# Optimization experiments

Measured on AMD Instinct MI355X. Metric: run time of the kernel, lower is better.

## Reference

```python
import jax, jax.numpy as jnp
import numpy as np

V_TH = 1.0  # spikingjelly IFNode default threshold; v starts at 0, hard reset after fire


def setup_inputs() -> dict:
    key = jax.random.key(0)
    k_x, k_w1, k_w2 = jax.random.split(key, 3)
    B, IN, FEAT, OUT = 4096, 3136, 6272, 500
    # binary input spikes (LatencyEncoder emits 0/1 spikes per timestep)
    x = (jax.random.uniform(k_x, (B, IN)) < 0.5).astype(jnp.float32)
    # Linear weights, torch layout [out_features, in_features], kaiming-ish scale
    W1 = jax.random.normal(k_w1, (FEAT, IN), dtype=jnp.float32) / np.sqrt(IN)
    W2 = jax.random.normal(k_w2, (OUT, FEAT), dtype=jnp.float32) / np.sqrt(FEAT)
    return {"x": x, "W1": W1, "W2": W2}


def reference(x, W1, W2):
    # Linear (no bias) -> IF neuron single step: v = 0 + I; spike = (v >= V_TH); hard reset
    v1 = x @ W1.T                      # [B, FEAT]
    s1 = (v1 >= V_TH).astype(x.dtype)  # binary hidden spikes
    v2 = s1 @ W2.T                     # [B, OUT]
    s2 = (v2 >= V_TH).astype(x.dtype)  # output spikes
    return s2
```

## Files before the change

### kernel.cpp

```cpp
#include <hip/hip_runtime.h>


namespace {
constexpr int kB = 4096;
constexpr int kIn = 3136;
constexpr int kFeat = 6272;
constexpr int kFeatWords = 196;
constexpr int kOut = 500;
constexpr size_t kPlane1 = (size_t)kFeat * kIn;
constexpr size_t kW1F = 3 * kPlane1;
constexpr size_t kW2F = (size_t)784 * 12288;
constexpr size_t kS1Bytes = (size_t)kB * kFeatWords * 4;
constexpr size_t kXb2Bytes = (size_t)49 * kB * 8;
constexpr unsigned kCap1 = 2u << 20;
constexpr unsigned kCap2 = 1u << 16;
__device__ constexpr double kTau1 = 7.4769e-4;
__device__ constexpr double kTau2 = 1.4955e-3;
}

typedef int v4i __attribute__((ext_vector_type(4)));
typedef int v16i __attribute__((ext_vector_type(16)));

__device__ __forceinline__ void gload_lds16(const void* g, void* l) {
  __builtin_amdgcn_global_load_lds((__attribute__((address_space(1))) void*)(g),
                                   (__attribute__((address_space(3))) void*)(l),
                                   16, 0, 0);
}

__device__ __forceinline__ v4i expand16(unsigned b) {
  unsigned u0 = (((b      ) & 0xFu) * 0x204081u) & 0x01010101u;
  unsigned u1 = (((b >> 4 ) & 0xFu) * 0x204081u) & 0x01010101u;
  unsigned u2 = (((b >> 8 ) & 0xFu) * 0x204081u) & 0x01010101u;
  unsigned u3 = (((b >> 12) & 0xFu) * 0x204081u) & 0x01010101u;
  return (v4i){(int)u0, (int)u1, (int)u2, (int)u3};
}

__device__ __forceinline__ void split3(float w, signed char* d) {
  float c = rintf(w * 128.f);
  d[0] = (signed char)(int)c;
  float r = fmaf(c, -7.8125e-03f, w);
  c = rintf(r * 16384.f);
  d[1] = (signed char)(int)c;
  r = fmaf(c, -6.103515625e-05f, r);
  c = rintf(r * 2097152.f);
  d[2] = (signed char)(int)c;
}

__global__ __launch_bounds__(256) void conv_w1F(const float* __restrict__ W,
                                                signed char* __restrict__ F) {
  const int bx = blockIdx.x;
  const int fb = bx / 49;
  const int kt = bx % 49;
  const int f = threadIdx.x & 63;
  const int g = threadIdx.x >> 6;
  const float* src = W + (size_t)(fb * 64 + f) * kIn + kt * 64 + g * 16;
  union { signed char c[16]; int4 v; } o[3];
#pragma unroll
  for (int q = 0; q < 4; ++q) {
    const float4 w = *(const float4*)(src + q * 4);
    signed char d[4][3];
    split3(w.x, d[0]); split3(w.y, d[1]); split3(w.z, d[2]); split3(w.w, d[3]);
#pragma unroll
    for (int e = 0; e < 4; ++e)
#pragma unroll
      for (int j = 0; j < 3; ++j) o[j].c[q * 4 + e] = d[e][j];
  }
#pragma unroll
  for (int j = 0; j < 3; ++j)
    *(int4*)(F + ((size_t)bx * 3 + j) * 4096 + g * 1024 + f * 16) = o[j].v;
}

__global__ __launch_bounds__(256) void conv_w2F(const float* __restrict__ W,
                                                signed char* __restrict__ F) {
  const int bx = blockIdx.x;
  const int fb = bx / 98;
  const int kt = bx % 98;
  const int f = threadIdx.x & 63;
  const int g = threadIdx.x >> 6;
  const int feat = fb * 64 + f;
  union { signed char c[16]; int4 v; } o[3];
#pragma unroll
  for (int q = 0; q < 4; ++q) {
    float4 w = {0.f, 0.f, 0.f, 0.f};
    if (feat < kOut)
      w = *(const float4*)(W + (size_t)feat * kFeat + kt * 64 + g * 16 + q * 4);
    signed char d[4][3];
    split3(w.x, d[0]); split3(w.y, d[1]); split3(w.z, d[2]); split3(w.w, d[3]);
#pragma unroll
    for (int e = 0; e < 4; ++e)
#pragma unroll
      for (int j = 0; j < 3; ++j) o[j].c[q * 4 + e] = d[e][j];
  }
#pragma unroll
  for (int j = 0; j < 3; ++j)
    *(int4*)(F + ((size_t)bx * 3 + j) * 4096 + g * 1024 + f * 16) = o[j].v;
}

__global__ __launch_bounds__(256) void pack_x2(const float* __restrict__ X,
                                               uint2* __restrict__ xb2) {
  const int wid = (blockIdx.x * 256 + threadIdx.x) >> 6;
  const int lane = threadIdx.x & 63;
  const int b = wid / 49;
  const int g = wid % 49;
  const float v = X[(size_t)b * kIn + g * 64 + lane];
  const unsigned long long bal = __ballot(v != 0.f);
  if (lane == 0) xb2[(size_t)g * kB + b] = make_uint2((unsigned)bal, (unsigned)(bal >> 32));
}

__global__ __launch_bounds__(512, 4) void fc1_v6(
    const uint2* __restrict__ xb2, const signed char* __restrict__ w1lF,
    unsigned* __restrict__ s1b, unsigned* __restrict__ s1T,
    unsigned* __restrict__ cnt, unsigned* __restrict__ list) {
  __shared__ __align__(16) signed char lds[24576];
  const int tid = threadIdx.x;
  const int lane = tid & 63;
  const int ln31 = lane & 31;
  const int half = lane >> 5;
  const int wv = tid >> 6;
  const int waveM = wv >> 1;
  const int waveN = wv & 1;
  const int bx = blockIdx.y;
  const int bM = blockIdx.x * 128;

  const signed char* const gbase = w1lF + (size_t)bx * 49 * 12288;
  const bool has1 = (wv < 4);
  const unsigned sG0 = wv * 1024u + lane * 16u;
  const unsigned sL0 = wv * 1024u;
  const unsigned sG1 = (wv + 8) * 1024u + lane * 16u;
  const unsigned sL1 = (wv + 8) * 1024u;

  const uint2* const aptr = xb2 + bM + waveM * 32 + ln31;
  const unsigned bfeat = (waveN * 32 + ln31) * 16u;

  v16i acc[3] = {};
  uint2 aC, aN;
  aC = aptr[0];
  gload_lds16(gbase + sG0, lds + sL0);
  if (has1) gload_lds16(gbase + sG1, lds + sL1);

  for (int kt = 0; kt < 49; ++kt) {
    __syncthreads();
    const int cb = (kt & 1) * 12288;
    if (kt < 48) {
      const int nb = ((kt + 1) & 1) * 12288;
      const size_t go = (size_t)(kt + 1) * 12288;
      gload_lds16(gbase + go + sG0, lds + nb + sL0);
      if (has1) gload_lds16(gbase + go + sG1, lds + nb + sL1);
      aN = aptr[(size_t)(kt + 1) * kB];
    }
#pragma unroll
    for (int kk = 0; kk < 2; ++kk) {
      const unsigned gsel = (kk * 2 + half) * 1024u;
      const v4i b0 = *(const v4i*)(lds + cb + 0 * 4096 + gsel + bfeat);
      const v4i b1 = *(const v4i*)(lds + cb + 1 * 4096 + gsel + bfeat);
      const v4i b2 = *(const v4i*)(lds + cb + 2 * 4096 + gsel + bfeat);
      const unsigned word = kk ? aC.y : aC.x;
      const v4i a = expand16((word >> (half * 16)) & 0xFFFFu);
      acc[0] = __builtin_amdgcn_mfma_i32_32x32x32_i8(a, b0, acc[0], 0, 0, 0);
      acc[1] = __builtin_amdgcn_mfma_i32_32x32x32_i8(a, b1, acc[1], 0, 0, 0);
      acc[2] = __builtin_amdgcn_mfma_i32_32x32x32_i8(a, b2, acc[2], 0, 0, 0);
    }
    aC = aN;
  }

  const double s7 = 0.0078125;
  const int word = bx * 2 + waveN;
  const int fcol = word * 32 + ln31;
#pragma unroll
  for (int t = 0; t < 16; ++t) {
    double v = (double)acc[2][t];
    v = v * s7 + (double)acc[1][t];
    v = v * s7 + (double)acc[0][t];
    v = v * s7;
    const unsigned long long bal = __ballot(v >= 1.0);
    const int mrow = bM + waveM * 32 + (t & 3) + 8 * (t >> 2);
    if (lane == 0) {
      s1b[(size_t)mrow * kFeatWords + word] = (unsigned)bal;
      s1T[(size_t)word * kB + mrow] = (unsigned)bal;
    }
    if (lane == 32) {
      s1b[(size_t)(mrow + 4) * kFeatWords + word] = (unsigned)(bal >> 32);
      s1T[(size_t)word * kB + mrow + 4] = (unsigned)(bal >> 32);
    }
    if (fabs(v - 1.0) <= kTau1) {
      const unsigned idx = atomicAdd(cnt, 1u);
      if (idx < kCap1) list[idx] = ((unsigned)(mrow + 4 * half) << 13) | (unsigned)fcol;
    }
  }
}

__global__ __launch_bounds__(256) void fc1_correct(
    const float* __restrict__ x, const float* __restrict__ W1,
    const unsigned* __restrict__ cnt, const unsigned* __restrict__ list,
    unsigned* __restrict__ s1b, unsigned* __restrict__ s1T) {
  const unsigned n = min(cnt[0], kCap1);
  const int lane = threadIdx.x & 63;
  const int wid = (blockIdx.x * 256 + threadIdx.x) >> 6;
  const int nw = (gridDim.x * 256) >> 6;
  for (unsigned i = wid; i < n; i += nw) {
    const unsigned u = list[i];
    const int b = (int)(u >> 13);
    const int f = (int)(u & 8191u);
    double s = 0.0;
    for (int k = lane; k < kIn; k += 64)
      s = fma((double)x[(size_t)b * kIn + k], (double)W1[(size_t)f * kIn + k], s);
#pragma unroll
    for (int off = 32; off > 0; off >>= 1) s += __shfl_down(s, off);
    if (lane == 0) {
      const unsigned mask = 1u << (f & 31);
      unsigned* p1 = s1b + (size_t)b * kFeatWords + (f >> 5);
      unsigned* p2 = s1T + (size_t)(f >> 5) * kB + b;
      if (s >= 1.0) { atomicOr(p1, mask); atomicOr(p2, mask); }
      else          { atomicAnd(p1, ~mask); atomicAnd(p2, ~mask); }
    }
  }
}

__global__ __launch_bounds__(128, 4) void fc2_v6(
    const unsigned* __restrict__ s1T, const signed char* __restrict__ w2lF,
    float* __restrict__ out, unsigned* __restrict__ cnt,
    unsigned* __restrict__ list) {
  const int tid = threadIdx.x;
  const int lane = tid & 63;
  const int ln31 = lane & 31;
  const int half = lane >> 5;
  const int wvN = tid >> 6;
  const int bx = blockIdx.y;
  const int bM = blockIdx.x * 32;

  const unsigned* const aptr = s1T + bM + ln31;
  const int fl = wvN * 32 + ln31;
  const signed char* const bbase =
      w2lF + (size_t)(bx * 98) * 12288 + half * 1024u + fl * 16u;

  v16i acc[3] = {};
  v4i b0[6], b1[6];
  uint2 a0, a1;

#define LOAD_TILE(nk, bf, ab)                                   \
  {                                                             \
    const signed char* bp = bbase + (size_t)(nk) * 12288;       \
    bf[0] = *(const v4i*)(bp);                                  \
    bf[1] = *(const v4i*)(bp + 2048);                           \
    bf[2] = *(const v4i*)(bp + 4096);                           \
    bf[3] = *(const v4i*)(bp + 6144);                           \
    bf[4] = *(const v4i*)(bp + 8192);                           \
    bf[5] = *(const v4i*)(bp + 10240);                          \
    (ab).x = aptr[(size_t)((nk) * 2) * kB];                     \
    (ab).y = aptr[(size_t)((nk) * 2 + 1) * kB];                 \
  }
#define COMPUTE_TILE(bf, ab)                                                    \
  {                                                                             \
    _Pragma("unroll")                                                           \
    for (int kk = 0; kk < 2; ++kk) {                                            \
      const unsigned word = kk ? (ab).y : (ab).x;                               \
      const v4i a = expand16((word >> (half * 16)) & 0xFFFFu);                  \
      acc[0] = __builtin_amdgcn_mfma_i32_32x32x32_i8(a, bf[kk], acc[0], 0,0,0); \
      acc[1] = __builtin_amdgcn_mfma_i32_32x32x32_i8(a, bf[2+kk], acc[1],0,0,0);\
      acc[2] = __builtin_amdgcn_mfma_i32_32x32x32_i8(a, bf[4+kk], acc[2],0,0,0);\
    }                                                                           \
  }

  LOAD_TILE(0, b0, a0);
  for (int kt = 0; kt + 2 <= 98; kt += 2) {
    LOAD_TILE(kt + 1, b1, a1);
    COMPUTE_TILE(b0, a0);
    const int nk2 = (kt + 2 < 98) ? kt + 2 : 97;
    LOAD_TILE(nk2, b0, a0);
    COMPUTE_TILE(b1, a1);
  }

  const double s7 = 0.0078125;
  const int o = bx * 64 + wvN * 32 + ln31;
#pragma unroll
  for (int t = 0; t < 16; ++t) {
    double v = (double)acc[2][t];
    v = v * s7 + (double)acc[1][t];
    v = v * s7 + (double)acc[0][t];
    v = v * s7;
    const int b = bM + (t & 3) + 8 * (t >> 2) + 4 * half;
    if (o < kOut) {
      out[(size_t)b * kOut + o] = (v >= 1.0) ? 1.0f : 0.0f;
      if (fabs(v - 1.0) <= kTau2) {
        const unsigned idx = atomicAdd(cnt, 1u);
        if (idx < kCap2) list[idx] = ((unsigned)b << 13) | (unsigned)o;
      }
    }
  }
#undef LOAD_TILE
#undef COMPUTE_TILE
}

__global__ __launch_bounds__(256) void fc2_correct(
    const unsigned* __restrict__ s1b, const float* __restrict__ W2,
    const unsigned* __restrict__ cnt, const unsigned* __restrict__ list,
    float* __restrict__ out) {
  const unsigned n = min(cnt[0], kCap2);
  const int lane = threadIdx.x & 63;
  const int wid = (blockIdx.x * 256 + threadIdx.x) >> 6;
  const int nw = (gridDim.x * 256) >> 6;
  for (unsigned i = wid; i < n; i += nw) {
    const unsigned u = list[i];
    const int b = (int)(u >> 13);
    const int o = (int)(u & 8191u);
    double s = 0.0;
    for (int k = lane; k < kFeat; k += 64) {
      const unsigned w = s1b[(size_t)b * kFeatWords + (k >> 5)];
      if ((w >> (k & 31)) & 1u) s += (double)W2[(size_t)o * kFeat + k];
    }
#pragma unroll
    for (int off = 32; off > 0; off >>= 1) s += __shfl_down(s, off);
    if (lane == 0) out[(size_t)b * kOut + o] = (s >= 1.0) ? 1.0f : 0.0f;
  }
}

__global__ __launch_bounds__(256) void snn_fc1(const float* __restrict__ x,
                                               const float* __restrict__ W1,
                                               unsigned int* __restrict__ s1bits) {
  __shared__ double Xd[32][66];
  __shared__ double Wd[32][66];
  __shared__ unsigned int spikes[64][2];
  const int tid = threadIdx.x;
  const int tx = tid & 15;
  const int ty = tid >> 4;
  const int b0 = blockIdx.y * 64;
  const int f0 = blockIdx.x * 64;
  if (tid < 128) spikes[tid >> 1][tid & 1] = 0u;
  double acc[4][4];
#pragma unroll
  for (int j = 0; j < 4; ++j)
#pragma unroll
    for (int i = 0; i < 4; ++i) acc[j][i] = 0.0;
  const int rl = tid >> 2;
  const int kq = (tid & 3) * 8;
  const float* xrow = x + (size_t)(b0 + rl) * kIn + kq;
  const float* wrow = W1 + (size_t)(f0 + rl) * kIn + kq;
  for (int kc = 0; kc < kIn; kc += 32) {
    const float4 xv0 = *(const float4*)(xrow + kc);
    const float4 xv1 = *(const float4*)(xrow + kc + 4);
    const float4 wv0 = *(const float4*)(wrow + kc);
    const float4 wv1 = *(const float4*)(wrow + kc + 4);
    __syncthreads();
    Xd[kq + 0][rl] = (double)xv0.x; Xd[kq + 1][rl] = (double)xv0.y;
    Xd[kq + 2][rl] = (double)xv0.z; Xd[kq + 3][rl] = (double)xv0.w;
    Xd[kq + 4][rl] = (double)xv1.x; Xd[kq + 5][rl] = (double)xv1.y;
    Xd[kq + 6][rl] = (double)xv1.z; Xd[kq + 7][rl] = (double)xv1.w;
    Wd[kq + 0][rl] = (double)wv0.x; Wd[kq + 1][rl] = (double)wv0.y;
    Wd[kq + 2][rl] = (double)wv0.z; Wd[kq + 3][rl] = (double)wv0.w;
    Wd[kq + 4][rl] = (double)wv1.x; Wd[kq + 5][rl] = (double)wv1.y;
    Wd[kq + 6][rl] = (double)wv1.z; Wd[kq + 7][rl] = (double)wv1.w;
    __syncthreads();
#pragma unroll
    for (int k = 0; k < 32; ++k) {
      const double2 xa = *(const double2*)&Xd[k][ty * 4];
      const double2 xb = *(const double2*)&Xd[k][ty * 4 + 2];
      const double2 wa = *(const double2*)&Wd[k][tx * 4];
      const double2 wb = *(const double2*)&Wd[k][tx * 4 + 2];
      const double xv[4] = {xa.x, xa.y, xb.x, xb.y};
      const double wv[4] = {wa.x, wa.y, wb.x, wb.y};
#pragma unroll
      for (int j = 0; j < 4; ++j)
#pragma unroll
        for (int i = 0; i < 4; ++i) acc[j][i] += xv[j] * wv[i];
    }
  }
  __syncthreads();
#pragma unroll
  for (int j = 0; j < 4; ++j) {
    unsigned int nib = 0u;
#pragma unroll
    for (int i = 0; i < 4; ++i) nib |= (acc[j][i] >= 1.0 ? 1u : 0u) << i;
    atomicOr(&spikes[ty * 4 + j][tx >> 3], nib << ((tx * 4) & 31));
  }
  __syncthreads();
  if (tid < 128) {
    const int r = tid >> 1;
    const int w = tid & 1;
    s1bits[(size_t)(b0 + r) * kFeatWords + (f0 >> 5) + w] = spikes[r][w];
  }
}

__global__ __launch_bounds__(256) void snn_fc2(const unsigned int* __restrict__ s1bits,
                                               const float* __restrict__ W2,
                                               float* __restrict__ out) {
  __shared__ double Wd[32][66];
  __shared__ unsigned int Sb[64];
  const int tid = threadIdx.x;
  const int tx = tid & 15;
  const int ty = tid >> 4;
  const int b0 = blockIdx.y * 64;
  const int o0 = blockIdx.x * 64;
  double acc[4][4];
#pragma unroll
  for (int j = 0; j < 4; ++j)
#pragma unroll
    for (int i = 0; i < 4; ++i) acc[j][i] = 0.0;
  const int rl = tid >> 2;
  const int kq = (tid & 3) * 8;
  int orow = o0 + rl;
  if (orow >= kOut) orow = kOut - 1;
  const float* wrow = W2 + (size_t)orow * kFeat + kq;
  for (int kc = 0; kc < kFeat; kc += 32) {
    const float4 wv0 = *(const float4*)(wrow + kc);
    const float4 wv1 = *(const float4*)(wrow + kc + 4);
    unsigned int sword = 0u;
    if (tid < 64) sword = s1bits[(size_t)(b0 + tid) * kFeatWords + (kc >> 5)];
    __syncthreads();
    Wd[kq + 0][rl] = (double)wv0.x; Wd[kq + 1][rl] = (double)wv0.y;
    Wd[kq + 2][rl] = (double)wv0.z; Wd[kq + 3][rl] = (double)wv0.w;
    Wd[kq + 4][rl] = (double)wv1.x; Wd[kq + 5][rl] = (double)wv1.y;
    Wd[kq + 6][rl] = (double)wv1.z; Wd[kq + 7][rl] = (double)wv1.w;
    if (tid < 64) Sb[tid] = sword;
    __syncthreads();
    const unsigned int rw0 = Sb[ty * 4 + 0];
    const unsigned int rw1 = Sb[ty * 4 + 1];
    const unsigned int rw2 = Sb[ty * 4 + 2];
    const unsigned int rw3 = Sb[ty * 4 + 3];
#pragma unroll
    for (int k = 0; k < 32; ++k) {
      const double2 wa = *(const double2*)&Wd[k][tx * 4];
      const double2 wb = *(const double2*)&Wd[k][tx * 4 + 2];
      const double wv[4] = {wa.x, wa.y, wb.x, wb.y};
      const double sv[4] = {(double)((rw0 >> k) & 1u), (double)((rw1 >> k) & 1u),
                            (double)((rw2 >> k) & 1u), (double)((rw3 >> k) & 1u)};
#pragma unroll
      for (int j = 0; j < 4; ++j)
#pragma unroll
        for (int i = 0; i < 4; ++i) acc[j][i] += sv[j] * wv[i];
    }
  }
#pragma unroll
  for (int j = 0; j < 4; ++j) {
    const int b = b0 + ty * 4 + j;
#pragma unroll
    for (int i = 0; i < 4; ++i) {
      const int o = o0 + tx * 4 + i;
      if (o < kOut) out[(size_t)b * kOut + o] = (acc[j][i] >= 1.0) ? 1.0f : 0.0f;
    }
  }
}

extern "C" void kernel_launch(void* const* d_in, const int* in_sizes, int n_in,
                              void* d_out, int out_size, void* d_ws, size_t ws_size,
                              hipStream_t stream) {
  const float* x = (const float*)d_in[0];
  const float* W1 = (const float*)d_in[1];
  const float* W2 = (const float*)d_in[2];
  float* out = (float*)d_out;

  char* p = (char*)d_ws;
  signed char* w1lF = (signed char*)p;   p += kW1F;
  signed char* w2lF = (signed char*)p;   p += kW2F;
  unsigned* s1b = (unsigned*)p;          p += kS1Bytes;
  unsigned* s1T = (unsigned*)p;          p += kS1Bytes;
  uint2* xb2 = (uint2*)p;                p += kXb2Bytes;
  unsigned* list1 = (unsigned*)p;        p += (size_t)kCap1 * 4;
  unsigned* list2 = (unsigned*)p;        p += (size_t)kCap2 * 4;
  unsigned* ctrs = (unsigned*)p;         p += 256;
  const size_t need = (size_t)(p - (char*)d_ws);

  if (ws_size >= need) {
    hipMemsetAsync(ctrs, 0, 32, stream);
    conv_w1F<<<4802, 256, 0, stream>>>(W1, w1lF);
    conv_w2F<<<784, 256, 0, stream>>>(W2, w2lF);
    pack_x2<<<50176, 256, 0, stream>>>(x, xb2);
    fc1_v6<<<dim3(32, 98), 512, 0, stream>>>(xb2, w1lF, s1b, s1T, ctrs, list1);
    fc1_correct<<<1024, 256, 0, stream>>>(x, W1, ctrs, list1, s1b, s1T);
    fc2_v6<<<dim3(128, 8), 128, 0, stream>>>(s1T, w2lF, out, ctrs + 4, list2);
    fc2_correct<<<64, 256, 0, stream>>>(s1b, W2, ctrs + 4, list2, out);
  } else {
    unsigned* s1 = (unsigned*)d_ws;
    snn_fc1<<<dim3(98, 64), 256, 0, stream>>>(x, W1, s1);
    snn_fc2<<<dim3(8, 64), 256, 0, stream>>>(s1, W2, out);
  }
}
```

Baseline: 585.7 us.

## Triple-buffer fc1 LDS pipeline with manual waitcnt and swizzle block order

Rewrites the fc1 main loop to use three LDS stages instead of two, issuing loads two tiles ahead and using explicit vmcnt waits plus a raw s_barrier instead of __syncthreads at the top of each iteration. It also raises MFMA issue priority with s_setprio and remaps block indices in both fc1 and fc2 so that consecutive blocks are spread across weight column tiles, aiming for better L2/XCD locality. The goal is to hide global-to-LDS latency and cut barrier stalls. In exchange it uses more LDS per block, which may reduce occupancy, and the hand-written wait counts are fragile.

```diff
diff --git a/kernel.cpp b/kernel.cpp
--- a/kernel.cpp
+++ b/kernel.cpp
@@ -107,11 +107,11 @@
   if (lane == 0) xb2[(size_t)g * kB + b] = make_uint2((unsigned)bal, (unsigned)(bal >> 32));
 }
 
-__global__ __launch_bounds__(512, 4) void fc1_v6(
+__global__ __launch_bounds__(512, 4) void fc1_v7(
     const uint2* __restrict__ xb2, const signed char* __restrict__ w1lF,
     unsigned* __restrict__ s1b, unsigned* __restrict__ s1T,
     unsigned* __restrict__ cnt, unsigned* __restrict__ list) {
-  __shared__ __align__(16) signed char lds[24576];
+  __shared__ __align__(16) signed char lds[36864];
   const int tid = threadIdx.x;
   const int lane = tid & 63;
   const int ln31 = lane & 31;
@@ -119,8 +119,11 @@
   const int wv = tid >> 6;
   const int waveM = wv >> 1;
   const int waveN = wv & 1;
-  const int bx = blockIdx.y;
-  const int bM = blockIdx.x * 128;
+
+  const int lin = blockIdx.x + 32 * blockIdx.y;
+  const int sw = (lin & 7) * 392 + (lin >> 3);
+  const int bx = sw >> 5;
+  const int bM = (sw & 31) * 128;
 
   const signed char* const gbase = w1lF + (size_t)bx * 49 * 12288;
   const bool has1 = (wv < 4);
@@ -134,34 +137,74 @@
 
   v16i acc[3] = {};
   uint2 aC, aN;
+
+#define FC1_TILE(CBC, AA)                                                     \
+  {                                                                           \
+    _Pragma("unroll")                                                         \
+    for (int kk = 0; kk < 2; ++kk) {                                          \
+      const unsigned gsel = (kk * 2 + half) * 1024u;                          \
+      const v4i b0 = *(const v4i*)(lds + (CBC) + 0 * 4096 + gsel + bfeat);    \
+      const v4i b1 = *(const v4i*)(lds + (CBC) + 1 * 4096 + gsel + bfeat);    \
+      const v4i b2 = *(const v4i*)(lds + (CBC) + 2 * 4096 + gsel + bfeat);    \
+      const unsigned word = kk ? (AA).y : (AA).x;                             \
+      const v4i a = expand16((word >> (half * 16)) & 0xFFFFu);                \
+      __builtin_amdgcn_s_setprio(1);                                          \
+      acc[0] = __builtin_amdgcn_mfma_i32_32x32x32_i8(a, b0, acc[0], 0, 0, 0); \
+      acc[1] = __builtin_amdgcn_mfma_i32_32x32x32_i8(a, b1, acc[1], 0, 0, 0); \
+      acc[2] = __builtin_amdgcn_mfma_i32_32x32x32_i8(a, b2, acc[2], 0, 0, 0); \
+      __builtin_amdgcn_s_setprio(0);                                          \
+    }                                                                         \
+  }
+
+#define FC1_STEP(CBC, SBC, AUSE, ALOAD)                                       \
+  {                                                                           \
+    ALOAD = *apre;                                                            \
+    apre += kB;                                                               \
+    gload_lds16(gstage + sG0, lds + (SBC) + sL0);                             \
+    if (has1) gload_lds16(gstage + sG1, lds + (SBC) + sL1);                   \
+    gstage += 12288;                                                          \
+    FC1_TILE(CBC, AUSE);                                                      \
+    if (has1) asm volatile("s_waitcnt vmcnt(3)" ::: "memory");                \
+    else      asm volatile("s_waitcnt vmcnt(2)" ::: "memory");                \
+    __builtin_amdgcn_s_barrier();                                             \
+    asm volatile("" ::: "memory");                                            \
+  }
+
   aC = aptr[0];
+  asm volatile("" ::: "memory");
   gload_lds16(gbase + sG0, lds + sL0);
   if (has1) gload_lds16(gbase + sG1, lds + sL1);
-
-  for (int kt = 0; kt < 49; ++kt) {
-    __syncthreads();
-    const int cb = (kt & 1) * 12288;
-    if (kt < 48) {
-      const int nb = ((kt + 1) & 1) * 12288;
-      const size_t go = (size_t)(kt + 1) * 12288;
-      gload_lds16(gbase + go + sG0, lds + nb + sL0);
-      if (has1) gload_lds16(gbase + go + sG1, lds + nb + sL1);
-      aN = aptr[(size_t)(kt + 1) * kB];
-    }
-#pragma unroll
-    for (int kk = 0; kk < 2; ++kk) {
-      const unsigned gsel = (kk * 2 + half) * 1024u;
-      const v4i b0 = *(const v4i*)(lds + cb + 0 * 4096 + gsel + bfeat);
-      const v4i b1 = *(const v4i*)(lds + cb + 1 * 4096 + gsel + bfeat);
-      const v4i b2 = *(const v4i*)(lds + cb + 2 * 4096 + gsel + bfeat);
-      const unsigned word = kk ? aC.y : aC.x;
-      const v4i a = expand16((word >> (half * 16)) & 0xFFFFu);
-      acc[0] = __builtin_amdgcn_mfma_i32_32x32x32_i8(a, b0, acc[0], 0, 0, 0);
-      acc[1] = __builtin_amdgcn_mfma_i32_32x32x32_i8(a, b1, acc[1], 0, 0, 0);
-      acc[2] = __builtin_amdgcn_mfma_i32_32x32x32_i8(a, b2, acc[2], 0, 0, 0);
-    }
-    aC = aN;
-  }
+  gload_lds16(gbase + 12288 + sG0, lds + 12288 + sL0);
+  if (has1) gload_lds16(gbase + 12288 + sG1, lds + 12288 + sL1);
+  if (has1) asm volatile("s_waitcnt vmcnt(2)" ::: "memory");
+  else      asm volatile("s_waitcnt vmcnt(1)" ::: "memory");
+  __builtin_amdgcn_s_barrier();
+  asm volatile("" ::: "memory");
+
+  const uint2* apre = aptr + (size_t)kB;
+  const signed char* gstage = gbase + 2 * 12288;
+
+  for (int t = 0; t < 7; ++t) {
+    FC1_STEP(0,     24576, aC, aN);
+    FC1_STEP(12288, 0,     aN, aC);
+    FC1_STEP(24576, 12288, aC, aN);
+    FC1_STEP(0,     24576, aN, aC);
+    FC1_STEP(12288, 0,     aC, aN);
+    FC1_STEP(24576, 12288, aN, aC);
+  }
+  FC1_STEP(0,     24576, aC, aN);
+  FC1_STEP(12288, 0,     aN, aC);
+  FC1_STEP(24576, 12288, aC, aN);
+  FC1_STEP(0,     24576, aN, aC);
+  FC1_STEP(12288, 0,     aC, aN);
+  aC = *apre;
+  FC1_TILE(24576, aN);
+  asm volatile("s_waitcnt vmcnt(0)" ::: "memory");
+  __builtin_amdgcn_s_barrier();
+  asm volatile("" ::: "memory");
+  FC1_TILE(0, aC);
+
+#undef FC1_STEP
 
   const double s7 = 0.0078125;
   const int word = bx * 2 + waveN;
@@ -187,6 +230,7 @@
       if (idx < kCap1) list[idx] = ((unsigned)(mrow + 4 * half) << 13) | (unsigned)fcol;
     }
   }
+#undef FC1_TILE
 }
 
 __global__ __launch_bounds__(256) void fc1_correct(
@@ -216,7 +260,7 @@
   }
 }
 
-__global__ __launch_bounds__(128, 4) void fc2_v6(
+__global__ __launch_bounds__(128, 4) void fc2_v7(
     const unsigned* __restrict__ s1T, const signed char* __restrict__ w2lF,
     float* __restrict__ out, unsigned* __restrict__ cnt,
     unsigned* __restrict__ list) {
@@ -225,8 +269,11 @@
   const int ln31 = lane & 31;
   const int half = lane >> 5;
   const int wvN = tid >> 6;
-  const int bx = blockIdx.y;
-  const int bM = blockIdx.x * 32;
+
+  const int lin = blockIdx.x + 128 * blockIdx.y;
+  const int sw = ((lin & 7) << 7) + (lin >> 3);
+  const int bx = sw >> 7;
+  const int bM = (sw & 127) * 32;
 
   const unsigned* const aptr = s1T + bM + ln31;
   const int fl = wvN * 32 + ln31;
@@ -464,9 +511,9 @@
     conv_w1F<<<4802, 256, 0, stream>>>(W1, w1lF);
     conv_w2F<<<784, 256, 0, stream>>>(W2, w2lF);
     pack_x2<<<50176, 256, 0, stream>>>(x, xb2);
-    fc1_v6<<<dim3(32, 98), 512, 0, stream>>>(xb2, w1lF, s1b, s1T, ctrs, list1);
+    fc1_v7<<<dim3(32, 98), 512, 0, stream>>>(xb2, w1lF, s1b, s1T, ctrs, list1);
     fc1_correct<<<1024, 256, 0, stream>>>(x, W1, ctrs, list1, s1b, s1T);
-    fc2_v6<<<dim3(128, 8), 128, 0, stream>>>(s1T, w2lF, out, ctrs + 4, list2);
+    fc2_v7<<<dim3(128, 8), 128, 0, stream>>>(s1T, w2lF, out, ctrs + 4, list2);
     fc2_correct<<<64, 256, 0, stream>>>(s1b, W2, ctrs + 4, list2, out);
   } else {
     unsigned* s1 = (unsigned*)d_ws;
```

After: 588.0 us. No clear change (+0.4%).

## Deepen fc1 LDS pipeline to four stages and swizzle block order

Applied to the files above, without the earlier changes.

fc1 now uses a 4-buffer LDS ring with three tiles in flight, in place of a double buffer with a full __syncthreads each step. It uses explicit vmcnt waits, raw barriers, and register prefetch of the next B fragments so LDS reads overlap the MFMAs. Both fc1 and fc2 remap their linear block index with a swizzle so that concurrently running blocks are spread across XCD-interleaved tiles, aiming at better L2 reuse. The change doubles LDS per block, which may lower occupancy. The hand-written waitcnt counts are fragile if the compiler reorders memory ops.

```diff
diff --git a/kernel.cpp b/kernel.cpp
--- a/kernel.cpp
+++ b/kernel.cpp
@@ -107,11 +107,11 @@
   if (lane == 0) xb2[(size_t)g * kB + b] = make_uint2((unsigned)bal, (unsigned)(bal >> 32));
 }
 
-__global__ __launch_bounds__(512, 4) void fc1_v6(
+__global__ __launch_bounds__(512, 4) void fc1_v8(
     const uint2* __restrict__ xb2, const signed char* __restrict__ w1lF,
     unsigned* __restrict__ s1b, unsigned* __restrict__ s1T,
     unsigned* __restrict__ cnt, unsigned* __restrict__ list) {
-  __shared__ __align__(16) signed char lds[24576];
+  __shared__ __align__(16) signed char lds[49152];
   const int tid = threadIdx.x;
   const int lane = tid & 63;
   const int ln31 = lane & 31;
@@ -119,8 +119,11 @@
   const int wv = tid >> 6;
   const int waveM = wv >> 1;
   const int waveN = wv & 1;
-  const int bx = blockIdx.y;
-  const int bM = blockIdx.x * 128;
+
+  const int lin = blockIdx.x + 32 * blockIdx.y;
+  const int sw = (lin & 7) * 392 + (lin >> 3);
+  const int bx = sw >> 5;
+  const int bM = (sw & 31) * 128;
 
   const signed char* const gbase = w1lF + (size_t)bx * 49 * 12288;
   const bool has1 = (wv < 4);
@@ -131,37 +134,82 @@
 
   const uint2* const aptr = xb2 + bM + waveM * 32 + ln31;
   const unsigned bfeat = (waveN * 32 + ln31) * 16u;
+  const unsigned g0sel = half * 1024u;
+  const unsigned g1sel = (2 + half) * 1024u;
 
   v16i acc[3] = {};
+  v4i bA0, bA1, bA2;
+  v4i bB0, bB1, bB2;
   uint2 aC, aN;
+
+#define FC1_PHASE(CB, PB, SB, AU, AL, SOFF, AOFF, DO_STAGE, DO_A, DO_PRE, WAITM) \
+  {                                                                           \
+    bB0 = *(const v4i*)(lds + (CB) + 0 * 4096 + g1sel + bfeat);               \
+    bB1 = *(const v4i*)(lds + (CB) + 1 * 4096 + g1sel + bfeat);               \
+    bB2 = *(const v4i*)(lds + (CB) + 2 * 4096 + g1sel + bfeat);               \
+    if (DO_STAGE) {                                                           \
+      gload_lds16(gstage + (SOFF) + sG0, lds + (SB) + sL0);                   \
+      if (has1) gload_lds16(gstage + (SOFF) + sG1, lds + (SB) + sL1);         \
+    }                                                                         \
+    if (DO_A) { (AL) = apre[(size_t)(AOFF)]; }                                \
+    {                                                                         \
+      const v4i a0 = expand16(((AU).x >> (half * 16)) & 0xFFFFu);             \
+      acc[0] = __builtin_amdgcn_mfma_i32_32x32x32_i8(a0, bA0, acc[0], 0,0,0); \
+      acc[1] = __builtin_amdgcn_mfma_i32_32x32x32_i8(a0, bA1, acc[1], 0,0,0); \
+      acc[2] = __builtin_amdgcn_mfma_i32_32x32x32_i8(a0, bA2, acc[2], 0,0,0); \
+      const v4i a1 = expand16(((AU).y >> (half * 16)) & 0xFFFFu);             \
+      acc[0] = __builtin_amdgcn_mfma_i32_32x32x32_i8(a1, bB0, acc[0], 0,0,0); \
+      acc[1] = __builtin_amdgcn_mfma_i32_32x32x32_i8(a1, bB1, acc[1], 0,0,0); \
+      acc[2] = __builtin_amdgcn_mfma_i32_32x32x32_i8(a1, bB2, acc[2], 0,0,0); \
+    }                                                                         \
+    if (DO_PRE) {                                                             \
+      bA0 = *(const v4i*)(lds + (PB) + 0 * 4096 + g0sel + bfeat);             \
+      bA1 = *(const v4i*)(lds + (PB) + 1 * 4096 + g0sel + bfeat);             \
+      bA2 = *(const v4i*)(lds + (PB) + 2 * 4096 + g0sel + bfeat);             \
+    }                                                                         \
+    if ((WAITM) == 0) {                                                       \
+      if (has1) asm volatile("s_waitcnt vmcnt(3)" ::: "memory");              \
+      else      asm volatile("s_waitcnt vmcnt(2)" ::: "memory");              \
+      __builtin_amdgcn_s_barrier();                                           \
+      asm volatile("" ::: "memory");                                          \
+    } else if ((WAITM) == 1) {                                                \
+      asm volatile("s_waitcnt vmcnt(2)" ::: "memory");                        \
+      __builtin_amdgcn_s_barrier();                                           \
+      asm volatile("" ::: "memory");                                          \
+    }                                                                         \
+  }
+
+  gload_lds16(gbase + 0 * 12288 + sG0, lds + 0 + sL0);
+  if (has1) gload_lds16(gbase + 0 * 12288 + sG1, lds + 0 + sL1);
+  gload_lds16(gbase + 1 * 12288 + sG0, lds + 12288 + sL0);
+  if (has1) gload_lds16(gbase + 1 * 12288 + sG1, lds + 12288 + sL1);
+  gload_lds16(gbase + 2 * 12288 + sG0, lds + 24576 + sL0);
+  if (has1) gload_lds16(gbase + 2 * 12288 + sG1, lds + 24576 + sL1);
   aC = aptr[0];
-  gload_lds16(gbase + sG0, lds + sL0);
-  if (has1) gload_lds16(gbase + sG1, lds + sL1);
-
-  for (int kt = 0; kt < 49; ++kt) {
-    __syncthreads();
-    const int cb = (kt & 1) * 12288;
-    if (kt < 48) {
-      const int nb = ((kt + 1) & 1) * 12288;
-      const size_t go = (size_t)(kt + 1) * 12288;
-      gload_lds16(gbase + go + sG0, lds + nb + sL0);
-      if (has1) gload_lds16(gbase + go + sG1, lds + nb + sL1);
-      aN = aptr[(size_t)(kt + 1) * kB];
-    }
-#pragma unroll
-    for (int kk = 0; kk < 2; ++kk) {
-      const unsigned gsel = (kk * 2 + half) * 1024u;
-      const v4i b0 = *(const v4i*)(lds + cb + 0 * 4096 + gsel + bfeat);
-      const v4i b1 = *(const v4i*)(lds + cb + 1 * 4096 + gsel + bfeat);
-      const v4i b2 = *(const v4i*)(lds + cb + 2 * 4096 + gsel + bfeat);
-      const unsigned word = kk ? aC.y : aC.x;
-      const v4i a = expand16((word >> (half * 16)) & 0xFFFFu);
-      acc[0] = __builtin_amdgcn_mfma_i32_32x32x32_i8(a, b0, acc[0], 0, 0, 0);
-      acc[1] = __builtin_amdgcn_mfma_i32_32x32x32_i8(a, b1, acc[1], 0, 0, 0);
-      acc[2] = __builtin_amdgcn_mfma_i32_32x32x32_i8(a, b2, acc[2], 0, 0, 0);
-    }
-    aC = aN;
-  }
+  asm volatile("s_waitcnt vmcnt(0)" ::: "memory");
+  __builtin_amdgcn_s_barrier();
+  asm volatile("" ::: "memory");
+  bA0 = *(const v4i*)(lds + 0 * 4096 + g0sel + bfeat);
+  bA1 = *(const v4i*)(lds + 1 * 4096 + g0sel + bfeat);
+  bA2 = *(const v4i*)(lds + 2 * 4096 + g0sel + bfeat);
+
+  const uint2* apre = aptr + (size_t)kB;
+  const signed char* gstage = gbase + 3 * 12288;
+
+  for (int t = 0; t < 11; ++t) {
+    FC1_PHASE(0,     12288, 36864, aC, aN, 0,         0,      1, 1, 1, 0);
+    FC1_PHASE(12288, 24576, 0,     aN, aC, 12288,     kB,     1, 1, 1, 0);
+    FC1_PHASE(24576, 36864, 12288, aC, aN, 2 * 12288, 2 * kB, 1, 1, 1, 0);
+    FC1_PHASE(36864, 0,     24576, aN, aC, 3 * 12288, 3 * kB, 1, 1, 1, 0);
+    gstage += 4 * 12288;
+    apre += (size_t)4 * kB;
+  }
+  FC1_PHASE(0,     12288, 36864, aC, aN, 0,     0,      1, 1, 1, 0);
+  FC1_PHASE(12288, 24576, 0,     aN, aC, 12288, kB,     1, 1, 1, 0);
+  FC1_PHASE(24576, 36864, 0,     aC, aN, 0,     2 * kB, 0, 1, 1, 1);
+  FC1_PHASE(36864, 0,     0,     aN, aC, 0,     3 * kB, 0, 1, 1, 2);
+  FC1_PHASE(0,     0,     0,     aC, aN, 0,     0,      0, 0, 0, 2);
+#undef FC1_PHASE
 
   const double s7 = 0.0078125;
   const int word = bx * 2 + waveN;
@@ -216,7 +264,7 @@
   }
 }
 
-__global__ __launch_bounds__(128, 4) void fc2_v6(
+__global__ __launch_bounds__(128, 4) void fc2_v7(
     const unsigned* __restrict__ s1T, const signed char* __restrict__ w2lF,
     float* __restrict__ out, unsigned* __restrict__ cnt,
     unsigned* __restrict__ list) {
@@ -225,8 +273,11 @@
   const int ln31 = lane & 31;
   const int half = lane >> 5;
   const int wvN = tid >> 6;
-  const int bx = blockIdx.y;
-  const int bM = blockIdx.x * 32;
+
+  const int lin = blockIdx.x + 128 * blockIdx.y;
+  const int sw = ((lin & 7) << 7) + (lin >> 3);
+  const int bx = sw >> 7;
+  const int bM = (sw & 127) * 32;
 
   const unsigned* const aptr = s1T + bM + ln31;
   const int fl = wvN * 32 + ln31;
@@ -464,9 +515,9 @@
     conv_w1F<<<4802, 256, 0, stream>>>(W1, w1lF);
     conv_w2F<<<784, 256, 0, stream>>>(W2, w2lF);
     pack_x2<<<50176, 256, 0, stream>>>(x, xb2);
-    fc1_v6<<<dim3(32, 98), 512, 0, stream>>>(xb2, w1lF, s1b, s1T, ctrs, list1);
+    fc1_v8<<<dim3(32, 98), 512, 0, stream>>>(xb2, w1lF, s1b, s1T, ctrs, list1);
     fc1_correct<<<1024, 256, 0, stream>>>(x, W1, ctrs, list1, s1b, s1T);
-    fc2_v6<<<dim3(128, 8), 128, 0, stream>>>(s1T, w2lF, out, ctrs + 4, list2);
+    fc2_v7<<<dim3(128, 8), 128, 0, stream>>>(s1T, w2lF, out, ctrs + 4, list2);
     fc2_correct<<<64, 256, 0, stream>>>(s1b, W2, ctrs + 4, list2, out);
   } else {
     unsigned* s1 = (unsigned*)d_ws;
```

New measurement: 587.0 us. No clear change (+0.2%).

## Stage three K-tiles per barrier in fc1 and swizzle block order in fc1/fc2

Applied to the files above, without the earlier changes.

The fc1 kernel now loads three 12 KB weight K-tiles into a larger double-buffered LDS region per iteration, cutting the number of barriers from 49 to 17 and issuing more async global-to-LDS loads per barrier. Both fc1 and fc2 remap their linear block index with a swizzle so that concurrently running blocks on different XCDs share weight or activation tiles, aiming for better L2 reuse. The larger LDS allocation (72 KB) may lower occupancy below the declared launch bound of 4 blocks.

```diff
diff --git a/kernel.cpp b/kernel.cpp
--- a/kernel.cpp
+++ b/kernel.cpp
@@ -107,11 +107,11 @@
   if (lane == 0) xb2[(size_t)g * kB + b] = make_uint2((unsigned)bal, (unsigned)(bal >> 32));
 }
 
-__global__ __launch_bounds__(512, 4) void fc1_v6(
+__global__ __launch_bounds__(512, 4) void fc1_v9(
     const uint2* __restrict__ xb2, const signed char* __restrict__ w1lF,
     unsigned* __restrict__ s1b, unsigned* __restrict__ s1T,
     unsigned* __restrict__ cnt, unsigned* __restrict__ list) {
-  __shared__ __align__(16) signed char lds[24576];
+  __shared__ __align__(16) signed char lds[73728];
   const int tid = threadIdx.x;
   const int lane = tid & 63;
   const int ln31 = lane & 31;
@@ -119,49 +119,83 @@
   const int wv = tid >> 6;
   const int waveM = wv >> 1;
   const int waveN = wv & 1;
-  const int bx = blockIdx.y;
-  const int bM = blockIdx.x * 128;
+
+  const int lin = blockIdx.x + 32 * blockIdx.y;
+  const int sw = (lin & 7) * 392 + (lin >> 3);
+  const int bx = sw >> 5;
+  const int bM = (sw & 31) * 128;
 
   const signed char* const gbase = w1lF + (size_t)bx * 49 * 12288;
-  const bool has1 = (wv < 4);
   const unsigned sG0 = wv * 1024u + lane * 16u;
   const unsigned sL0 = wv * 1024u;
-  const unsigned sG1 = (wv + 8) * 1024u + lane * 16u;
-  const unsigned sL1 = (wv + 8) * 1024u;
 
   const uint2* const aptr = xb2 + bM + waveM * 32 + ln31;
   const unsigned bfeat = (waveN * 32 + ln31) * 16u;
+  const unsigned gs0 = half * 1024u;
+  const unsigned gs1 = gs0 + 2048u;
 
   v16i acc[3] = {};
-  uint2 aC, aN;
-  aC = aptr[0];
+  uint2 aC0, aC1, aC2, aN0, aN1, aN2;
+
+#define FC1_KT(TB, AW)                                                        \
+  {                                                                           \
+    const v4i b0 = *(const v4i*)(lds + (TB) + 0 * 4096 + gs0 + bfeat);        \
+    const v4i b1 = *(const v4i*)(lds + (TB) + 1 * 4096 + gs0 + bfeat);        \
+    const v4i b2 = *(const v4i*)(lds + (TB) + 2 * 4096 + gs0 + bfeat);        \
+    const v4i a0 = expand16(((AW).x >> (half * 16)) & 0xFFFFu);               \
+    acc[0] = __builtin_amdgcn_mfma_i32_32x32x32_i8(a0, b0, acc[0], 0, 0, 0);  \
+    acc[1] = __builtin_amdgcn_mfma_i32_32x32x32_i8(a0, b1, acc[1], 0, 0, 0);  \
+    acc[2] = __builtin_amdgcn_mfma_i32_32x32x32_i8(a0, b2, acc[2], 0, 0, 0);  \
+    const v4i c0 = *(const v4i*)(lds + (TB) + 0 * 4096 + gs1 + bfeat);        \
+    const v4i c1 = *(const v4i*)(lds + (TB) + 1 * 4096 + gs1 + bfeat);        \
+    const v4i c2 = *(const v4i*)(lds + (TB) + 2 * 4096 + gs1 + bfeat);        \
+    const v4i a1 = expand16(((AW).y >> (half * 16)) & 0xFFFFu);               \
+    acc[0] = __builtin_amdgcn_mfma_i32_32x32x32_i8(a1, c0, acc[0], 0, 0, 0);  \
+    acc[1] = __builtin_amdgcn_mfma_i32_32x32x32_i8(a1, c1, acc[1], 0, 0, 0);  \
+    acc[2] = __builtin_amdgcn_mfma_i32_32x32x32_i8(a1, c2, acc[2], 0, 0, 0);  \
+  }
+
   gload_lds16(gbase + sG0, lds + sL0);
-  if (has1) gload_lds16(gbase + sG1, lds + sL1);
-
-  for (int kt = 0; kt < 49; ++kt) {
+  gload_lds16(gbase + 8192 + sG0, lds + 8192 + sL0);
+  gload_lds16(gbase + 16384 + sG0, lds + 16384 + sL0);
+  gload_lds16(gbase + 24576 + sG0, lds + 24576 + sL0);
+  if (wv < 4) gload_lds16(gbase + 32768 + sG0, lds + 32768 + sL0);
+  aC0 = aptr[0];
+  aC1 = aptr[(size_t)kB];
+  aC2 = aptr[(size_t)2 * kB];
+
+  for (int p = 0; p < 17; ++p) {
     __syncthreads();
-    const int cb = (kt & 1) * 12288;
-    if (kt < 48) {
-      const int nb = ((kt + 1) & 1) * 12288;
-      const size_t go = (size_t)(kt + 1) * 12288;
-      gload_lds16(gbase + go + sG0, lds + nb + sL0);
-      if (has1) gload_lds16(gbase + go + sG1, lds + nb + sL1);
-      aN = aptr[(size_t)(kt + 1) * kB];
-    }
-#pragma unroll
-    for (int kk = 0; kk < 2; ++kk) {
-      const unsigned gsel = (kk * 2 + half) * 1024u;
-      const v4i b0 = *(const v4i*)(lds + cb + 0 * 4096 + gsel + bfeat);
-      const v4i b1 = *(const v4i*)(lds + cb + 1 * 4096 + gsel + bfeat);
-      const v4i b2 = *(const v4i*)(lds + cb + 2 * 4096 + gsel + bfeat);
-      const unsigned word = kk ? aC.y : aC.x;
-      const v4i a = expand16((word >> (half * 16)) & 0xFFFFu);
-      acc[0] = __builtin_amdgcn_mfma_i32_32x32x32_i8(a, b0, acc[0], 0, 0, 0);
-      acc[1] = __builtin_amdgcn_mfma_i32_32x32x32_i8(a, b1, acc[1], 0, 0, 0);
-      acc[2] = __builtin_amdgcn_mfma_i32_32x32x32_i8(a, b2, acc[2], 0, 0, 0);
-    }
-    aC = aN;
-  }
+    const int cb = (p & 1) * 36864;
+    if (p < 16) {
+      const int nb = ((p + 1) & 1) * 36864;
+      const size_t go = (size_t)(p + 1) * 36864;
+      if (p < 15) {
+        gload_lds16(gbase + go + sG0, lds + nb + sL0);
+        gload_lds16(gbase + go + 8192 + sG0, lds + nb + 8192 + sL0);
+        gload_lds16(gbase + go + 16384 + sG0, lds + nb + 16384 + sL0);
+        gload_lds16(gbase + go + 24576 + sG0, lds + nb + 24576 + sL0);
+        if (wv < 4) gload_lds16(gbase + go + 32768 + sG0, lds + nb + 32768 + sL0);
+      } else {
+        gload_lds16(gbase + go + sG0, lds + nb + sL0);
+        if (wv < 4) gload_lds16(gbase + go + 8192 + sG0, lds + nb + 8192 + sL0);
+      }
+      const int k1 = 3 * p + 4 < 49 ? 3 * p + 4 : 48;
+      const int k2 = 3 * p + 5 < 49 ? 3 * p + 5 : 48;
+      aN0 = aptr[(size_t)(3 * p + 3) * kB];
+      aN1 = aptr[(size_t)k1 * kB];
+      aN2 = aptr[(size_t)k2 * kB];
+    }
+    FC1_KT(cb, aC0);
+    if (p < 16) {
+      FC1_KT(cb + 12288, aC1);
+      FC1_KT(cb + 24576, aC2);
+    }
+    aC0 = aN0;
+    aC1 = aN1;
+    aC2 = aN2;
+  }
+#undef FC1_KT
 
   const double s7 = 0.0078125;
   const int word = bx * 2 + waveN;
@@ -216,7 +250,7 @@
   }
 }
 
-__global__ __launch_bounds__(128, 4) void fc2_v6(
+__global__ __launch_bounds__(128, 4) void fc2_v7(
     const unsigned* __restrict__ s1T, const signed char* __restrict__ w2lF,
     float* __restrict__ out, unsigned* __restrict__ cnt,
     unsigned* __restrict__ list) {
@@ -225,8 +259,11 @@
   const int ln31 = lane & 31;
   const int half = lane >> 5;
   const int wvN = tid >> 6;
-  const int bx = blockIdx.y;
-  const int bM = blockIdx.x * 32;
+
+  const int lin = blockIdx.x + 128 * blockIdx.y;
+  const int sw = ((lin & 7) << 7) + (lin >> 3);
+  const int bx = sw >> 7;
+  const int bM = (sw & 127) * 32;
 
   const unsigned* const aptr = s1T + bM + ln31;
   const int fl = wvN * 32 + ln31;
@@ -464,9 +501,9 @@
     conv_w1F<<<4802, 256, 0, stream>>>(W1, w1lF);
     conv_w2F<<<784, 256, 0, stream>>>(W2, w2lF);
     pack_x2<<<50176, 256, 0, stream>>>(x, xb2);
-    fc1_v6<<<dim3(32, 98), 512, 0, stream>>>(xb2, w1lF, s1b, s1T, ctrs, list1);
+    fc1_v9<<<dim3(32, 98), 512, 0, stream>>>(xb2, w1lF, s1b, s1T, ctrs, list1);
     fc1_correct<<<1024, 256, 0, stream>>>(x, W1, ctrs, list1, s1b, s1T);
-    fc2_v6<<<dim3(128, 8), 128, 0, stream>>>(s1T, w2lF, out, ctrs + 4, list2);
+    fc2_v7<<<dim3(128, 8), 128, 0, stream>>>(s1T, w2lF, out, ctrs + 4, list2);
     fc2_correct<<<64, 256, 0, stream>>>(s1b, W2, ctrs + 4, list2, out);
   } else {
     unsigned* s1 = (unsigned*)d_ws;
```

Measured after the change: 574.1 us. -2.0%, faster.
